# Performance work log

Hardware: AMD Instinct MI355X
Metric: run time of the kernel (lower is better)

The kernel has to match this reference:

```python
import jax, jax.numpy as jnp
import numpy as np

N_HEADS = 16
WINDOW = 128
EPS = 1e-6
NEG_INF = -1e30  # effectively -inf after softmax in fp32


def setup_inputs() -> dict:
    key = jax.random.key(0)
    ks = jax.random.split(key, 5)
    B, T, D = 2, 2048, 1024
    scale = 1.0 / np.sqrt(D)
    return {
        "x": jax.random.normal(ks[0], (B, T, D), dtype=jnp.float32),
        "Wq": jax.random.normal(ks[1], (D, D), dtype=jnp.float32) * scale,
        "Wk": jax.random.normal(ks[2], (D, D), dtype=jnp.float32) * scale,
        "Wv": jax.random.normal(ks[3], (D, D), dtype=jnp.float32) * scale,
        "Wo": jax.random.normal(ks[4], (D, D), dtype=jnp.float32) * scale,
    }


def _l2norm(t):
    # torch F.normalize: t / max(||t||, eps)
    n = jnp.sqrt(jnp.sum(t * t, axis=-1, keepdims=True))
    return t / jnp.maximum(n, EPS)


def reference(x, Wq, Wk, Wv, Wo):
    B, T, D = x.shape
    H, hd = N_HEADS, D // N_HEADS
    # projections (torch Linear: x @ W.T), split heads -> [B, H, T, hd]
    def proj(W):
        return jnp.einsum('btd,ed->bte', x, W).reshape(B, T, H, hd).transpose(0, 2, 1, 3)
    q = _l2norm(proj(Wq))
    k = _l2norm(proj(Wk))
    v = proj(Wv)
    # scores [B, H, T, T] (no 1/sqrt(d) scale in the source)
    attn = jnp.einsum('bhqd,bhkd->bhqk', q, k)
    pos = jnp.arange(T)
    rel = pos[None, :] - pos[:, None]            # rel[i, j] = j - i
    mask = (rel < 0) | (rel >= WINDOW)           # allowed: 0 <= j-i < window
    base = jnp.linspace(0.0, 1.0, H, dtype=x.dtype)
    slopes = jnp.power(jnp.asarray(2.0, x.dtype), -(8.0 * base))  # [H]
    alibi = -jnp.abs(rel).astype(x.dtype)[None, :, :] * slopes[:, None, None]  # [H,T,T]
    bias = jnp.where(mask[None, :, :], jnp.asarray(NEG_INF, x.dtype), alibi)
    attn = jax.nn.softmax(attn + bias[None], axis=-1)
    out = jnp.einsum('bhqk,bhkd->bhqd', attn, v)
    out = out.transpose(0, 2, 1, 3).reshape(B, T, D)
    return jnp.einsum('btd,ed->bte', out, Wo)
```

## Files before the change

kernel.cpp:

```cpp
#include <hip/hip_runtime.h>
#include <hip/hip_bf16.h>

#define T_SEQ   2048
#define BATCH   2
#define DMODEL  1024
#define NHEADS  16
#define HDIM    64
#define WINDOW  128

typedef __attribute__((ext_vector_type(8))) short bf16x8;
typedef __attribute__((ext_vector_type(4))) float f32x4;

#define LGKM(n)  asm volatile("s_waitcnt lgkmcnt(" #n ")" ::: "memory")
#define VMCNT(n) asm volatile("s_waitcnt vmcnt(" #n ")" ::: "memory")
#define SCHEDB() __builtin_amdgcn_sched_barrier(0)
#define BAR()    __builtin_amdgcn_s_barrier()

__device__ inline void gld_lds16(const __hip_bfloat16* g, __hip_bfloat16* l) {
    __builtin_amdgcn_global_load_lds(
        (const __attribute__((address_space(1))) unsigned int*)g,
        (__attribute__((address_space(3))) unsigned int*)l, 16, 0, 0);
}

__device__ inline bf16x8 ds_readb128(const __hip_bfloat16* p) {
    bf16x8 r;
    asm volatile("ds_read_b128 %0, %1"
                 : "=v"(r)
                 : "v"((const __attribute__((address_space(3))) __hip_bfloat16*)p));
    return r;
}

__global__ __launch_bounds__(256) void cvt_kernel(
    const float* __restrict__ x,  const float* __restrict__ Wq,
    const float* __restrict__ Wk, const float* __restrict__ Wv,
    const float* __restrict__ Wo,
    __hip_bfloat16* __restrict__ xb, __hip_bfloat16* __restrict__ Wb)
{
    const int lid = blockIdx.x;
    const float* src;
    __hip_bfloat16* dst;
    int blk;
    if (lid < 2048) { src = x; dst = xb; blk = lid; }
    else {
        int slot = (lid - 2048) >> 9;
        blk = (lid - 2048) & 511;
        src = (slot == 0) ? Wq : (slot == 1) ? Wk : (slot == 2) ? Wv : Wo;
        dst = Wb + (size_t)slot * 1024 * 1024;
    }
    int i = (blk * 256 + threadIdx.x) * 8;
    float4 a = *(const float4*)(src + i);
    float4 b = *(const float4*)(src + i + 4);
    __hip_bfloat16 pk[8] = {
        __float2bfloat16(a.x), __float2bfloat16(a.y),
        __float2bfloat16(a.z), __float2bfloat16(a.w),
        __float2bfloat16(b.x), __float2bfloat16(b.y),
        __float2bfloat16(b.z), __float2bfloat16(b.w)};
    *(uint4*)(dst + i) = *(uint4*)pk;
}

__global__ __launch_bounds__(256, 2) void gemm_qkv(
    const __hip_bfloat16* __restrict__ A,
    const __hip_bfloat16* __restrict__ Wp,
    __hip_bfloat16* __restrict__ C0,
    __hip_bfloat16* __restrict__ C1,
    __hip_bfloat16* __restrict__ C2)
{
    const int lid   = blockIdx.x;
    const int wgid  = (lid & 7) * 96 + (lid >> 3);
    const int bn    = wgid % 24;
    const int bm    = wgid / 24;
    const int m0    = bm * 128;
    const int n0    = bn * 128;
    const int z     = n0 >> 10;
    const int cbase = n0 & 1023;

    __shared__ __hip_bfloat16 S[2][2][128 * 64];

    const int t    = threadIdx.x;
    const int lane = t & 63;
    const int wv   = t >> 6;
    const int lrow = lane & 15;
    const int quad = lane >> 4;
    const int wm   = (wv >> 1) * 64;
    const int wn   = (wv & 1) * 64;
    const int drow = lane >> 3;
    const int sl   = lane & 7;

    f32x4 acc[4][4];
#pragma unroll
    for (int i = 0; i < 4; ++i)
#pragma unroll
        for (int j = 0; j < 4; ++j)
            acc[i][j] = (f32x4){0.f, 0.f, 0.f, 0.f};

    auto STAGE = [&](int tile, int buf) {
        const int k0 = tile << 6;
#pragma unroll
        for (int inst = 0; inst < 4; ++inst) {
            int r0 = wv * 32 + inst * 8;
            int r  = r0 + drow;
            int gcx = (sl - r) & 7;
            gld_lds16(A + (size_t)(m0 + r) * DMODEL + k0 + gcx * 8,
                      &S[buf][0][r0 * 64]);
        }
#pragma unroll
        for (int inst = 0; inst < 4; ++inst) {
            int r0 = wv * 32 + inst * 8;
            int r  = r0 + drow;
            int gcx = (sl - r) & 7;
            gld_lds16(Wp + (size_t)(n0 + r) * DMODEL + k0 + gcx * 8,
                      &S[buf][1][r0 * 64]);
        }
    };

    auto RDA = [&](int buf, int mi, int kc) -> bf16x8 {
        int r = wm + mi * 16 + lrow;
        return ds_readb128(&S[buf][0][r * 64 + (((kc + r) & 7) << 3)]);
    };
    auto RDB = [&](int buf, int ni, int kc) -> bf16x8 {
        int r = wn + ni * 16 + lrow;
        return ds_readb128(&S[buf][1][r * 64 + (((kc + r) & 7) << 3)]);
    };

    bf16x8 a0[4], b0[4], a1[4], b1[4];

    STAGE(0, 0);
    VMCNT(0);
    BAR();
#pragma unroll
    for (int mi = 0; mi < 4; ++mi) a0[mi] = RDA(0, mi, quad);
#pragma unroll
    for (int ni = 0; ni < 4; ++ni) b0[ni] = RDB(0, ni, quad);

#pragma unroll 2
    for (int tt = 0; tt < 16; ++tt) {
        const int cur = tt & 1, nxt = cur ^ 1;
        if (tt < 15) STAGE(tt + 1, nxt);
#pragma unroll
        for (int mi = 0; mi < 4; ++mi) a1[mi] = RDA(cur, mi, 4 + quad);
#pragma unroll
        for (int ni = 0; ni < 4; ++ni) b1[ni] = RDB(cur, ni, 4 + quad);
        LGKM(8); SCHEDB();
        __builtin_amdgcn_s_setprio(1);
#pragma unroll
        for (int mi = 0; mi < 4; ++mi)
#pragma unroll
            for (int ni = 0; ni < 4; ++ni)
                acc[mi][ni] = __builtin_amdgcn_mfma_f32_16x16x32_bf16(
                    a0[mi], b0[ni], acc[mi][ni], 0, 0, 0);
        __builtin_amdgcn_s_setprio(0);
        VMCNT(0);
        LGKM(0); SCHEDB();
        BAR();
        if (tt < 15) {
#pragma unroll
            for (int mi = 0; mi < 4; ++mi) a0[mi] = RDA(nxt, mi, quad);
#pragma unroll
            for (int ni = 0; ni < 4; ++ni) b0[ni] = RDB(nxt, ni, quad);
        }
        __builtin_amdgcn_s_setprio(1);
#pragma unroll
        for (int mi = 0; mi < 4; ++mi)
#pragma unroll
            for (int ni = 0; ni < 4; ++ni)
                acc[mi][ni] = __builtin_amdgcn_mfma_f32_16x16x32_bf16(
                    a1[mi], b1[ni], acc[mi][ni], 0, 0, 0);
        __builtin_amdgcn_s_setprio(0);
    }

    if (z != 2) {
#pragma unroll
        for (int mi = 0; mi < 4; ++mi) {
#pragma unroll
            for (int rr = 0; rr < 4; ++rr) {
                float ss = 0.f;
#pragma unroll
                for (int ni = 0; ni < 4; ++ni)
                    ss += acc[mi][ni][rr] * acc[mi][ni][rr];
                ss += __shfl_xor(ss, 1);
                ss += __shfl_xor(ss, 2);
                ss += __shfl_xor(ss, 4);
                ss += __shfl_xor(ss, 8);
                float inv = 1.0f / fmaxf(sqrtf(ss), 1e-6f);
#pragma unroll
                for (int ni = 0; ni < 4; ++ni)
                    acc[mi][ni][rr] *= inv;
            }
        }
    }

    __hip_bfloat16* C = (z == 0) ? C0 : (z == 1) ? C1 : C2;
#pragma unroll
    for (int mi = 0; mi < 4; ++mi) {
#pragma unroll
        for (int rr = 0; rr < 4; ++rr) {
            int row = m0 + wm + mi * 16 + quad * 4 + rr;
            __hip_bfloat16* Crow = C + (size_t)row * DMODEL + cbase + wn + lrow;
#pragma unroll
            for (int ni = 0; ni < 4; ++ni)
                Crow[ni * 16] = __float2bfloat16(acc[mi][ni][rr]);
        }
    }
}

__global__ __launch_bounds__(256, 2) void gemm_o(
    const __hip_bfloat16* __restrict__ A,
    const __hip_bfloat16* __restrict__ W,
    float* __restrict__ C)
{
    const int lid  = blockIdx.x;
    const int wgid = (lid & 7) * 32 + (lid >> 3);
    const int bn   = wgid & 7;
    const int bm   = wgid >> 3;
    const int m0   = bm * 128;
    const int n0   = bn * 128;

    __shared__ __hip_bfloat16 S[4][2][128 * 32];

    const int t    = threadIdx.x;
    const int lane = t & 63;
    const int wv   = t >> 6;
    const int lrow = lane & 15;
    const int quad = lane >> 4;
    const int wm   = (wv >> 1) * 64;
    const int wn   = (wv & 1) * 64;

    f32x4 acc[4][4];
#pragma unroll
    for (int i = 0; i < 4; ++i)
#pragma unroll
        for (int j = 0; j < 4; ++j)
            acc[i][j] = (f32x4){0.f, 0.f, 0.f, 0.f};

    auto STAGE = [&](int h) {
        const int slot = h & 3;
        const int k0   = h * 32;
        const int r    = (lane >> 2);
        const int c    = lane & 3;
#pragma unroll
        for (int i = 0; i < 2; ++i) {
            int row0 = i * 64 + wv * 16;
            int row  = row0 + r;
            int gcx  = (c - (row >> 1)) & 3;
            gld_lds16(A + (size_t)(m0 + row) * DMODEL + k0 + gcx * 8,
                      &S[slot][0][row0 * 32]);
        }
#pragma unroll
        for (int i = 0; i < 2; ++i) {
            int row0 = i * 64 + wv * 16;
            int row  = row0 + r;
            int gcx  = (c - (row >> 1)) & 3;
            gld_lds16(W + (size_t)(n0 + row) * DMODEL + k0 + gcx * 8,
                      &S[slot][1][row0 * 32]);
        }
    };

    auto RD = [&](const __hip_bfloat16* base, int r) -> bf16x8 {
        return ds_readb128(base + r * 32 + (((quad + (r >> 1)) & 3) << 3));
    };

    bf16x8 a_[2][4], b_[2][4];

#define READS_O(P, H) { \
    const __hip_bfloat16* Sa = &S[(H) & 3][0][0]; \
    const __hip_bfloat16* Sb = &S[(H) & 3][1][0]; \
    _Pragma("unroll") for (int mi = 0; mi < 4; ++mi) \
        a_[P][mi] = RD(Sa, wm + mi * 16 + lrow); \
    _Pragma("unroll") for (int ni = 0; ni < 4; ++ni) \
        b_[P][ni] = RD(Sb, wn + ni * 16 + lrow); }

#define OBODY(H, P, PN, DO_STAGE, DO_READS, GATE) { \
    if (DO_STAGE) STAGE((H) + 3); \
    if (DO_READS) READS_O(PN, (H) + 1); \
    GATE; SCHEDB(); \
    __builtin_amdgcn_s_setprio(1); \
    _Pragma("unroll") for (int mi = 0; mi < 4; ++mi) \
    _Pragma("unroll") for (int ni = 0; ni < 4; ++ni) \
        acc[mi][ni] = __builtin_amdgcn_mfma_f32_16x16x32_bf16( \
            a_[P][mi], b_[P][ni], acc[mi][ni], 0, 0, 0); \
    __builtin_amdgcn_s_setprio(0); \
    VMCNT(4); BAR(); }

    STAGE(0); STAGE(1); STAGE(2);
    VMCNT(4);
    BAR();
    READS_O(0, 0);

    for (int it = 0; it < 15; ++it) {
        const int h = it * 2;
        OBODY(h,     0, 1, true,      true, LGKM(8));
        OBODY(h + 1, 1, 0, (it < 14), true, LGKM(8));
    }
    OBODY(30, 0, 1, false, true,  LGKM(8));
    OBODY(31, 1, 0, false, false, LGKM(0));

#undef OBODY
#undef READS_O

#pragma unroll
    for (int mi = 0; mi < 4; ++mi) {
#pragma unroll
        for (int rr = 0; rr < 4; ++rr) {
            int row = m0 + wm + mi * 16 + quad * 4 + rr;
            float* Crow = C + (size_t)row * DMODEL + n0 + wn + lrow;
#pragma unroll
            for (int ni = 0; ni < 4; ++ni)
                Crow[ni * 16] = acc[mi][ni][rr];
        }
    }
}

__global__ __launch_bounds__(512) void attn_kernel(
    const __hip_bfloat16* __restrict__ Q,
    const __hip_bfloat16* __restrict__ K,
    const __hip_bfloat16* __restrict__ V,
    __hip_bfloat16* __restrict__ O)
{
    const int qb = blockIdx.x * 128;
    const int h  = blockIdx.y;
    const int b  = blockIdx.z;

    __shared__ __hip_bfloat16 KsP[8 * 16 * 168];
    __shared__ __hip_bfloat16 Vt[64 * 264];

    const size_t base = ((size_t)b * T_SEQ) * DMODEL + h * HDIM;
    const int t    = threadIdx.x;
    const int lane = t & 63;
    const int w    = t >> 6;

    {
        const int drow = lane >> 3, sl = lane & 7;
#pragma unroll
        for (int inst = 0; inst < 4; inst++) {
            int r0 = w * 32 + inst * 8;
            int r  = r0 + drow;
            int gcx = (sl - r) & 7;
            int j  = min(qb + r, T_SEQ - 1);
            gld_lds16(K + base + (size_t)j * DMODEL + gcx * 8, &KsP[r0 * 64]);
        }
    }
    if (t < 256) {
        int c  = t & 7;
        int b0 = t >> 3;
        int sg = (b0 & ~7) | ((b0 + c) & 7);
        unsigned short m[8][8];
#pragma unroll
        for (int i = 0; i < 8; i++) {
            int j = min(qb + b0 * 8 + i, T_SEQ - 1);
            uint4 u = *(const uint4*)(V + base + (size_t)j * DMODEL + c * 8);
            unsigned short tmp[8];
            *(uint4*)tmp = u;
#pragma unroll
            for (int e = 0; e < 8; e++) m[e][i] = tmp[e];
        }
#pragma unroll
        for (int e = 0; e < 8; e++)
            *(uint4*)&Vt[(c * 8 + e) * 264 + sg * 8] = *(uint4*)m[e];
    }
    if (t < 64) {
        uint4 zz = {0, 0, 0, 0};
        *(uint4*)&Vt[t * 264 + 256] = zz;
    }
    __syncthreads();

    const int col  = lane & 15;
    const int quad = lane >> 4;
    const float slope = exp2f(-8.0f * (float)h / 15.0f);

    const __hip_bfloat16* qp = Q + base + (size_t)(qb + w * 16 + col) * DMODEL + quad * 8;
    bf16x8 qf0 = *(const bf16x8*)(qp);
    bf16x8 qf1 = *(const bf16x8*)(qp + 32);

    f32x4 sc[9];
#pragma unroll
    for (int kt = 0; kt < 9; kt++) {
        sc[kt] = (f32x4){0.f, 0.f, 0.f, 0.f};
        int r = w * 16 + kt * 16 + col;
        bf16x8 kb0 = *(const bf16x8*)&KsP[r * 64 + ((quad     + r) & 7) * 8];
        bf16x8 kb1 = *(const bf16x8*)&KsP[r * 64 + ((quad + 4 + r) & 7) * 8];
        sc[kt] = __builtin_amdgcn_mfma_f32_16x16x32_bf16(qf0, kb0, sc[kt], 0, 0, 0);
        sc[kt] = __builtin_amdgcn_mfma_f32_16x16x32_bf16(qf1, kb1, sc[kt], 0, 0, 0);
    }

    float mx[4] = {-3e38f, -3e38f, -3e38f, -3e38f};
#pragma unroll
    for (int kt = 0; kt < 9; kt++) {
#pragma unroll
        for (int r = 0; r < 4; r++) {
            int ql  = quad * 4 + r;
            int rel = kt * 16 + col - ql;
            int ka  = qb + w * 16 + kt * 16 + col;
            bool valid = (rel >= 0) && (rel < WINDOW) && (ka < T_SEQ);
            float v = valid ? (sc[kt][r] - (float)rel * slope) : -1e30f;
            sc[kt][r] = v;
            mx[r] = fmaxf(mx[r], v);
        }
    }
#pragma unroll
    for (int r = 0; r < 4; r++) {
        mx[r] = fmaxf(mx[r], __shfl_xor(mx[r], 1));
        mx[r] = fmaxf(mx[r], __shfl_xor(mx[r], 2));
        mx[r] = fmaxf(mx[r], __shfl_xor(mx[r], 4));
        mx[r] = fmaxf(mx[r], __shfl_xor(mx[r], 8));
    }
    float sm[4] = {0.f, 0.f, 0.f, 0.f};
#pragma unroll
    for (int kt = 0; kt < 9; kt++) {
#pragma unroll
        for (int r = 0; r < 4; r++) {
            float e = __expf(sc[kt][r] - mx[r]);
            sc[kt][r] = e;
            sm[r] += e;
        }
    }
#pragma unroll
    for (int r = 0; r < 4; r++) {
        sm[r] += __shfl_xor(sm[r], 1);
        sm[r] += __shfl_xor(sm[r], 2);
        sm[r] += __shfl_xor(sm[r], 4);
        sm[r] += __shfl_xor(sm[r], 8);
        sm[r] = 1.0f / sm[r];
    }

    __syncthreads();
    __hip_bfloat16* Ps = KsP + w * (16 * 168);
#pragma unroll
    for (int kt = 0; kt < 9; kt++)
#pragma unroll
        for (int r = 0; r < 4; r++)
            Ps[(quad * 4 + r) * 168 + kt * 16 + col] = __float2bfloat16(sc[kt][r] * sm[r]);
#pragma unroll
    for (int i = 0; i < 4; i++)
        Ps[(lane & 15) * 168 + 144 + quad * 4 + i] = __float2bfloat16(0.f);
    __syncthreads();

    f32x4 o[4];
#pragma unroll
    for (int nd = 0; nd < 4; nd++) o[nd] = (f32x4){0.f, 0.f, 0.f, 0.f};
#pragma unroll
    for (int kc = 0; kc < 5; kc++) {
        bf16x8 pf = *(const bf16x8*)&Ps[col * 168 + kc * 32 + quad * 8];
        int bblk = w * 2 + kc * 4 + quad;
#pragma unroll
        for (int nd = 0; nd < 4; nd++) {
            int d  = nd * 16 + col;
            int sg = (bblk < 32) ? ((bblk & ~7) | ((bblk + (d >> 3)) & 7)) : 32;
            bf16x8 vf = *(const bf16x8*)&Vt[d * 264 + sg * 8];
            o[nd] = __builtin_amdgcn_mfma_f32_16x16x32_bf16(pf, vf, o[nd], 0, 0, 0);
        }
    }

#pragma unroll
    for (int r = 0; r < 4; r++) {
        __hip_bfloat16* op = O + base + (size_t)(qb + w * 16 + quad * 4 + r) * DMODEL + col;
#pragma unroll
        for (int nd = 0; nd < 4; nd++)
            op[nd * 16] = __float2bfloat16(o[nd][r]);
    }
}

extern "C" void kernel_launch(void* const* d_in, const int* in_sizes, int n_in,
                              void* d_out, int out_size, void* d_ws, size_t ws_size,
                              hipStream_t stream)
{
    const float* x  = (const float*)d_in[0];
    const float* Wq = (const float*)d_in[1];
    const float* Wk = (const float*)d_in[2];
    const float* Wv = (const float*)d_in[3];
    const float* Wo = (const float*)d_in[4];
    float* out = (float*)d_out;

    const size_t MT = (size_t)BATCH * T_SEQ;
    __hip_bfloat16* Qw = (__hip_bfloat16*)d_ws;
    __hip_bfloat16* Kw = Qw + MT * DMODEL;
    __hip_bfloat16* Vw = Kw + MT * DMODEL;
    __hip_bfloat16* XA = Vw + MT * DMODEL;
    __hip_bfloat16* Wb = XA + MT * DMODEL;

    cvt_kernel<<<4096, 256, 0, stream>>>(x, Wq, Wk, Wv, Wo, XA, Wb);

    gemm_qkv<<<dim3(768), 256, 0, stream>>>(XA, Wb, Qw, Kw, Vw);

    dim3 g2(T_SEQ / 128, NHEADS, BATCH);
    attn_kernel<<<g2, 512, 0, stream>>>(Qw, Kw, Vw, XA);

    gemm_o<<<dim3(256), 256, 0, stream>>>(XA, Wb + 3 * 1024 * 1024, out);
}
```

Baseline: 151.8 us.

## Restructure output GEMM to double-buffered BK=64 and split V transpose across all threads

Result: no change. 150.7 us (-0.7%).

```diff
diff --git a/kernel.cpp b/kernel.cpp
--- a/kernel.cpp
+++ b/kernel.cpp
@@ -215,7 +215,7 @@
     const int m0   = bm * 128;
     const int n0   = bn * 128;
 
-    __shared__ __hip_bfloat16 S[4][2][128 * 32];
+    __shared__ __hip_bfloat16 S[2][2][128 * 64];
 
     const int t    = threadIdx.x;
     const int lane = t & 63;
@@ -224,6 +224,8 @@
     const int quad = lane >> 4;
     const int wm   = (wv >> 1) * 64;
     const int wn   = (wv & 1) * 64;
+    const int drow = lane >> 3;
+    const int sl   = lane & 7;
 
     f32x4 acc[4][4];
 #pragma unroll
@@ -232,70 +234,80 @@
         for (int j = 0; j < 4; ++j)
             acc[i][j] = (f32x4){0.f, 0.f, 0.f, 0.f};
 
-    auto STAGE = [&](int h) {
-        const int slot = h & 3;
-        const int k0   = h * 32;
-        const int r    = (lane >> 2);
-        const int c    = lane & 3;
-#pragma unroll
-        for (int i = 0; i < 2; ++i) {
-            int row0 = i * 64 + wv * 16;
-            int row  = row0 + r;
-            int gcx  = (c - (row >> 1)) & 3;
-            gld_lds16(A + (size_t)(m0 + row) * DMODEL + k0 + gcx * 8,
-                      &S[slot][0][row0 * 32]);
-        }
-#pragma unroll
-        for (int i = 0; i < 2; ++i) {
-            int row0 = i * 64 + wv * 16;
-            int row  = row0 + r;
-            int gcx  = (c - (row >> 1)) & 3;
-            gld_lds16(W + (size_t)(n0 + row) * DMODEL + k0 + gcx * 8,
-                      &S[slot][1][row0 * 32]);
+    auto STAGE = [&](int tile, int buf) {
+        const int k0 = tile << 6;
+#pragma unroll
+        for (int inst = 0; inst < 4; ++inst) {
+            int r0 = wv * 32 + inst * 8;
+            int r  = r0 + drow;
+            int gcx = (sl - r) & 7;
+            gld_lds16(A + (size_t)(m0 + r) * DMODEL + k0 + gcx * 8,
+                      &S[buf][0][r0 * 64]);
+        }
+#pragma unroll
+        for (int inst = 0; inst < 4; ++inst) {
+            int r0 = wv * 32 + inst * 8;
+            int r  = r0 + drow;
+            int gcx = (sl - r) & 7;
+            gld_lds16(W + (size_t)(n0 + r) * DMODEL + k0 + gcx * 8,
+                      &S[buf][1][r0 * 64]);
         }
     };
 
-    auto RD = [&](const __hip_bfloat16* base, int r) -> bf16x8 {
-        return ds_readb128(base + r * 32 + (((quad + (r >> 1)) & 3) << 3));
+    auto RDA = [&](int buf, int mi, int kc) -> bf16x8 {
+        int r = wm + mi * 16 + lrow;
+        return ds_readb128(&S[buf][0][r * 64 + (((kc + r) & 7) << 3)]);
     };
-
-    bf16x8 a_[2][4], b_[2][4];
-
-#define READS_O(P, H) { \
-    const __hip_bfloat16* Sa = &S[(H) & 3][0][0]; \
-    const __hip_bfloat16* Sb = &S[(H) & 3][1][0]; \
-    _Pragma("unroll") for (int mi = 0; mi < 4; ++mi) \
-        a_[P][mi] = RD(Sa, wm + mi * 16 + lrow); \
-    _Pragma("unroll") for (int ni = 0; ni < 4; ++ni) \
-        b_[P][ni] = RD(Sb, wn + ni * 16 + lrow); }
-
-#define OBODY(H, P, PN, DO_STAGE, DO_READS, GATE) { \
-    if (DO_STAGE) STAGE((H) + 3); \
-    if (DO_READS) READS_O(PN, (H) + 1); \
-    GATE; SCHEDB(); \
-    __builtin_amdgcn_s_setprio(1); \
-    _Pragma("unroll") for (int mi = 0; mi < 4; ++mi) \
-    _Pragma("unroll") for (int ni = 0; ni < 4; ++ni) \
-        acc[mi][ni] = __builtin_amdgcn_mfma_f32_16x16x32_bf16( \
-            a_[P][mi], b_[P][ni], acc[mi][ni], 0, 0, 0); \
-    __builtin_amdgcn_s_setprio(0); \
-    VMCNT(4); BAR(); }
-
-    STAGE(0); STAGE(1); STAGE(2);
-    VMCNT(4);
+    auto RDB = [&](int buf, int ni, int kc) -> bf16x8 {
+        int r = wn + ni * 16 + lrow;
+        return ds_readb128(&S[buf][1][r * 64 + (((kc + r) & 7) << 3)]);
+    };
+
+    bf16x8 a0[4], b0[4], a1[4], b1[4];
+
+    STAGE(0, 0);
+    VMCNT(0);
     BAR();
-    READS_O(0, 0);
-
-    for (int it = 0; it < 15; ++it) {
-        const int h = it * 2;
-        OBODY(h,     0, 1, true,      true, LGKM(8));
-        OBODY(h + 1, 1, 0, (it < 14), true, LGKM(8));
-    }
-    OBODY(30, 0, 1, false, true,  LGKM(8));
-    OBODY(31, 1, 0, false, false, LGKM(0));
-
-#undef OBODY
-#undef READS_O
+#pragma unroll
+    for (int mi = 0; mi < 4; ++mi) a0[mi] = RDA(0, mi, quad);
+#pragma unroll
+    for (int ni = 0; ni < 4; ++ni) b0[ni] = RDB(0, ni, quad);
+
+#pragma unroll 2
+    for (int tt = 0; tt < 16; ++tt) {
+        const int cur = tt & 1, nxt = cur ^ 1;
+        if (tt < 15) STAGE(tt + 1, nxt);
+#pragma unroll
+        for (int mi = 0; mi < 4; ++mi) a1[mi] = RDA(cur, mi, 4 + quad);
+#pragma unroll
+        for (int ni = 0; ni < 4; ++ni) b1[ni] = RDB(cur, ni, 4 + quad);
+        LGKM(8); SCHEDB();
+        __builtin_amdgcn_s_setprio(1);
+#pragma unroll
+        for (int mi = 0; mi < 4; ++mi)
+#pragma unroll
+            for (int ni = 0; ni < 4; ++ni)
+                acc[mi][ni] = __builtin_amdgcn_mfma_f32_16x16x32_bf16(
+                    a0[mi], b0[ni], acc[mi][ni], 0, 0, 0);
+        __builtin_amdgcn_s_setprio(0);
+        VMCNT(0);
+        LGKM(0); SCHEDB();
+        BAR();
+        if (tt < 15) {
+#pragma unroll
+            for (int mi = 0; mi < 4; ++mi) a0[mi] = RDA(nxt, mi, quad);
+#pragma unroll
+            for (int ni = 0; ni < 4; ++ni) b0[ni] = RDB(nxt, ni, quad);
+        }
+        __builtin_amdgcn_s_setprio(1);
+#pragma unroll
+        for (int mi = 0; mi < 4; ++mi)
+#pragma unroll
+            for (int ni = 0; ni < 4; ++ni)
+                acc[mi][ni] = __builtin_amdgcn_mfma_f32_16x16x32_bf16(
+                    a1[mi], b1[ni], acc[mi][ni], 0, 0, 0);
+        __builtin_amdgcn_s_setprio(0);
+    }
 
 #pragma unroll
     for (int mi = 0; mi < 4; ++mi) {
@@ -327,6 +339,8 @@
     const int t    = threadIdx.x;
     const int lane = t & 63;
     const int w    = t >> 6;
+    const int col  = lane & 15;
+    const int quad = lane >> 4;
 
     {
         const int drow = lane >> 3, sl = lane & 7;
@@ -339,14 +353,20 @@
             gld_lds16(K + base + (size_t)j * DMODEL + gcx * 8, &KsP[r0 * 64]);
         }
     }
-    if (t < 256) {
+
+    const __hip_bfloat16* qp = Q + base + (size_t)(qb + w * 16 + col) * DMODEL + quad * 8;
+    bf16x8 qf0 = *(const bf16x8*)(qp);
+    bf16x8 qf1 = *(const bf16x8*)(qp + 32);
+
+    {
         int c  = t & 7;
-        int b0 = t >> 3;
+        int b0 = (t >> 3) & 31;
+        int hf = t >> 8;
         int sg = (b0 & ~7) | ((b0 + c) & 7);
-        unsigned short m[8][8];
-#pragma unroll
-        for (int i = 0; i < 8; i++) {
-            int j = min(qb + b0 * 8 + i, T_SEQ - 1);
+        unsigned short m[8][4];
+#pragma unroll
+        for (int i = 0; i < 4; i++) {
+            int j = min(qb + b0 * 8 + hf * 4 + i, T_SEQ - 1);
             uint4 u = *(const uint4*)(V + base + (size_t)j * DMODEL + c * 8);
             unsigned short tmp[8];
             *(uint4*)tmp = u;
@@ -355,7 +375,7 @@
         }
 #pragma unroll
         for (int e = 0; e < 8; e++)
-            *(uint4*)&Vt[(c * 8 + e) * 264 + sg * 8] = *(uint4*)m[e];
+            *(uint2*)&Vt[(c * 8 + e) * 264 + sg * 8 + hf * 4] = *(uint2*)m[e];
     }
     if (t < 64) {
         uint4 zz = {0, 0, 0, 0};
@@ -363,13 +383,7 @@
     }
     __syncthreads();
 
-    const int col  = lane & 15;
-    const int quad = lane >> 4;
     const float slope = exp2f(-8.0f * (float)h / 15.0f);
-
-    const __hip_bfloat16* qp = Q + base + (size_t)(qb + w * 16 + col) * DMODEL + quad * 8;
-    bf16x8 qf0 = *(const bf16x8*)(qp);
-    bf16x8 qf1 = *(const bf16x8*)(qp + 32);
 
     f32x4 sc[9];
 #pragma unroll
```
